# Kernel optimization log

Measured on AMD Instinct MI355X. Metric: run time of the kernel, lower is better.

Reference implementation:

```python
import jax, jax.numpy as jnp
import numpy as np

N = 200000
E = 500000
F_IN = 165
HID = 256
N_CLASSES = 2


def setup_inputs() -> dict:
    key = jax.random.key(0)
    ks = jax.random.split(key, 8)
    x = jax.random.normal(ks[0], (N, F_IN), dtype=jnp.float32)
    edge_index = jax.random.randint(ks[1], (2, E), 0, N, dtype=jnp.int64)
    # PyG SAGEConv params: lin_l applied to mean-aggregated neighbors (with bias),
    # lin_r applied to root features (no bias). Glorot-ish init scale.
    def lin(k, fin, fout):
        return jax.random.normal(k, (fin, fout), dtype=jnp.float32) / np.sqrt(fin)
    return {
        "x": x,
        "edge_index": edge_index,
        "w1_l": lin(ks[2], F_IN, HID),
        "w1_r": lin(ks[3], F_IN, HID),
        "b1": jnp.zeros((HID,), dtype=jnp.float32),
        "w2_l": lin(ks[4], HID, N_CLASSES),
        "w2_r": lin(ks[5], HID, N_CLASSES),
        "b2": jnp.zeros((N_CLASSES,), dtype=jnp.float32),
    }


def _sage_conv(x, edge_index, w_l, w_r, b):
    # PyG SAGEConv with default mean aggregation:
    #   out = lin_l(mean_{j in N(i)} x_j) + lin_r(x_i) + b
    src, dst = edge_index[0], edge_index[1]
    n = x.shape[0]
    deg = jax.ops.segment_sum(jnp.ones((src.shape[0],), x.dtype), dst, num_segments=n)
    agg = jax.ops.segment_sum(x[src], dst, num_segments=n)  # [N, F]
    agg = agg / jnp.maximum(deg, 1.0)[:, None]
    return agg @ w_l + x @ w_r + b


def reference(x, edge_index, w1_l, w1_r, b1, w2_l, w2_r, b2):
    h = jax.nn.relu(_sage_conv(x, edge_index, w1_l, w1_r, b1))
    # F.dropout(training=self.training) is identity in eval mode.
    logits = _sage_conv(h, edge_index, w2_l, w2_r, b2)
    return (logits, edge_index)
```

## Files before the change

### kernel.cpp

```cpp
#include <hip/hip_runtime.h>
#include <hip/hip_bf16.h>
#include <hip/hip_fp16.h>

#define N_NODES 200000
#define N_EDGES 500000
#define F_IN    165
#define HID     256
#define SX      192
#define NB      782

typedef float    floatx4 __attribute__((ext_vector_type(4)));
typedef float    floatx4a __attribute__((ext_vector_type(4), aligned(16)));
typedef float    float4u __attribute__((ext_vector_type(4), aligned(4)));
typedef _Float16 half8   __attribute__((ext_vector_type(8)));

__global__ void cast_x_kernel(const float* __restrict__ x, half8* __restrict__ xh8) {
    int idx = blockIdx.x * blockDim.x + threadIdx.x;
    int row = idx / 24;
    int p = idx - row * 24;
    int f0 = p * 8;
    const float* px = x + (long)row * F_IN + f0;
    half8 r;
    if (f0 + 8 <= F_IN) {
        float4u lo = *(const float4u*)px;
        float4u hi = *(const float4u*)(px + 4);
#pragma unroll
        for (int q = 0; q < 4; ++q) r[q] = (_Float16)lo[q];
#pragma unroll
        for (int q = 0; q < 4; ++q) r[4 + q] = (_Float16)hi[q];
    } else {
#pragma unroll
        for (int q = 0; q < 8; ++q)
            r[q] = (f0 + q < F_IN) ? (_Float16)px[q] : (_Float16)0.0f;
    }
    xh8[idx] = r;
}

__global__ void hist_kernel(const int* __restrict__ ei, int* __restrict__ degi) {
    int e = blockIdx.x * blockDim.x + threadIdx.x;
    if (e < N_EDGES) atomicAdd(&degi[ei[N_EDGES + e]], 1);
}

__global__ __launch_bounds__(256) void block_sum_kernel(const int* __restrict__ degi,
                                                        int* __restrict__ bsum) {
    __shared__ int sh[256];
    int t = threadIdx.x, i = blockIdx.x * 256 + t;
    sh[t] = (i < N_NODES) ? degi[i] : 0;
    __syncthreads();
#pragma unroll
    for (int off = 128; off > 0; off >>= 1) {
        if (t < off) sh[t] += sh[t + off];
        __syncthreads();
    }
    if (t == 0) bsum[blockIdx.x] = sh[0];
}

__global__ __launch_bounds__(1024) void scan_bsum_kernel(const int* __restrict__ bsum,
                                                         int* __restrict__ boff,
                                                         int* __restrict__ row_start) {
    __shared__ int sh[1024];
    int t = threadIdx.x;
    int v = (t < NB) ? bsum[t] : 0;
    sh[t] = v;
    __syncthreads();
    for (int off = 1; off < 1024; off <<= 1) {
        int u = (t >= off) ? sh[t - off] : 0;
        __syncthreads();
        sh[t] += u;
        __syncthreads();
    }
    if (t < NB) boff[t] = sh[t] - v;
    if (t == 1023) row_start[N_NODES] = sh[1023];
}

__global__ __launch_bounds__(256) void scan_emit_kernel(const int* __restrict__ degi,
                                                        const int* __restrict__ boff,
                                                        int* __restrict__ row_start,
                                                        int* __restrict__ cursor,
                                                        float* __restrict__ invdeg) {
    __shared__ int sh[256];
    int t = threadIdx.x, i = blockIdx.x * 256 + t;
    int d = (i < N_NODES) ? degi[i] : 0;
    sh[t] = d;
    __syncthreads();
#pragma unroll
    for (int off = 1; off < 256; off <<= 1) {
        int u = (t >= off) ? sh[t - off] : 0;
        __syncthreads();
        sh[t] += u;
        __syncthreads();
    }
    if (i < N_NODES) {
        int row = boff[blockIdx.x] + sh[t] - d;
        row_start[i] = row;
        cursor[i] = row;
        invdeg[i] = 1.0f / fmaxf((float)d, 1.0f);
    }
}

__global__ void scatter_edges_kernel(const int* __restrict__ ei,
                                     int* __restrict__ cursor,
                                     int* __restrict__ csr) {
    int e = blockIdx.x * blockDim.x + threadIdx.x;
    if (e >= N_EDGES) return;
    int s = ei[e];
    int d = ei[N_EDGES + e];
    int pos = atomicAdd(&cursor[d], 1);
    csr[pos] = s;
}

__global__ void gather_agg_kernel(const half8* __restrict__ xh8,
                                  const int* __restrict__ row_start,
                                  const int* __restrict__ csr,
                                  half8* __restrict__ aggh8) {
    int idx = blockIdx.x * blockDim.x + threadIdx.x;
    int n = idx / 24;
    int p = idx - n * 24;
    int e0 = row_start[n], e1 = row_start[n + 1];
    half8 acc = {0, 0, 0, 0, 0, 0, 0, 0};
    half8 acc2 = {0, 0, 0, 0, 0, 0, 0, 0};
    int e = e0;
    for (; e + 2 <= e1; e += 2) {
        int s0 = csr[e], s1 = csr[e + 1];
        half8 v0 = xh8[(long)s0 * 24 + p];
        half8 v1 = xh8[(long)s1 * 24 + p];
        acc += v0;
        acc2 += v1;
    }
    if (e < e1) acc += xh8[(long)csr[e] * 24 + p];
    aggh8[idx] = acc + acc2;
}

__global__ void prep_bfrag_kernel(const float* __restrict__ w1l,
                                  const float* __restrict__ w1r,
                                  _Float16* __restrict__ bfrag) {
    int gid = blockIdx.x * blockDim.x + threadIdx.x;
    if (gid >= 12 * 16 * 64) return;
    int lane = gid & 63;
    int j = (gid >> 6) & 15;
    int c = gid >> 10;
    int quad = lane >> 4, n = lane & 15;
    const float* w = (c < 6) ? w1l : w1r;
    int kb = (c < 6 ? c : c - 6) * 32;
    int col = j * 16 + n;
    half8 r;
#pragma unroll
    for (int q = 0; q < 8; ++q) {
        int k = kb + quad * 8 + q;
        r[q] = (_Float16)((k < F_IN) ? w[k * HID + col] : 0.0f);
    }
    *(half8*)(bfrag + gid * 8) = r;
}

__global__ __launch_bounds__(512, 2) void gemm_fused_kernel(
        const _Float16* __restrict__ xh, const _Float16* __restrict__ aggh,
        const float* __restrict__ invdeg, const _Float16* __restrict__ bfrag,
        const float* __restrict__ b1,
        const float* __restrict__ w2l, const float* __restrict__ w2r,
        float* __restrict__ tl, float* __restrict__ tr) {
    __shared__ __attribute__((aligned(16))) _Float16 As[2][128 * 32];
    __shared__ float tlr[128][4];
    const int tid = threadIdx.x;
    const int w = tid >> 6, lane = tid & 63;
    const int quad = lane >> 4, l15 = lane & 15;
    const int rowbase = blockIdx.x * 128;
    const int mrow0 = rowbase + (w & 1) * 64;
    const int rhalf = (w & 1) * 64;
    const int jbase = (w >> 1) * 4;

    ((float*)tlr)[tid < 512 ? tid : 0] = 0.0f;

    const int srow_l = tid >> 2;
    const int sseg = (tid & 3) ^ ((srow_l >> 1) & 3);
    int srow = rowbase + srow_l;
    if (srow >= N_NODES) srow = N_NODES - 1;
    const long sgoff = (long)srow * SX + sseg * 8;

    floatx4 acc[4][4];
#pragma unroll
    for (int i = 0; i < 4; ++i)
#pragma unroll
        for (int jj = 0; jj < 4; ++jj)
            acc[i][jj] = (floatx4){0.f, 0.f, 0.f, 0.f};

    __syncthreads();

#pragma unroll 1
    for (int it = 0; it < 6; ++it) {
#pragma unroll
        for (int u = 0; u < 2; ++u) {
            const int cc = it * 2 + u;
            const _Float16* __restrict__ src = (cc < 6) ? aggh : xh;
            const int kb = (cc < 6 ? cc : cc - 6) * 32;
            const _Float16* gp = src + sgoff + kb;
            char* dst = (char*)(&As[u][0]) + (tid & ~63) * 16;
            __builtin_amdgcn_global_load_lds(
                (const __attribute__((address_space(1))) void*)gp,
                (__attribute__((address_space(3))) void*)dst, 16, 0, 0);
        }
        __syncthreads();

#pragma unroll
        for (int u = 0; u < 2; ++u) {
            const int cc = it * 2 + u;
            half8 a[4], b[4];
#pragma unroll
            for (int i = 0; i < 4; ++i) {
                int r = rhalf + i * 16 + l15;
                int slot = r * 4 + (quad ^ ((r >> 1) & 3));
                a[i] = *(const half8*)(&As[u][slot * 8]);
            }
#pragma unroll
            for (int jj = 0; jj < 4; ++jj)
                b[jj] = *(const half8*)(bfrag + (((cc * 16) + jbase + jj) * 64 + lane) * 8);
#pragma unroll
            for (int i = 0; i < 4; ++i)
#pragma unroll
                for (int jj = 0; jj < 4; ++jj)
                    acc[i][jj] = __builtin_amdgcn_mfma_f32_16x16x32_f16(a[i], b[jj], acc[i][jj], 0, 0, 0);

            if (cc == 5) {
#pragma unroll
                for (int i = 0; i < 4; ++i) {
                    int rb = mrow0 + i * 16 + quad * 4;
                    floatx4 iv;
                    if (rb + 3 < N_NODES) {
                        iv = *(const floatx4a*)(invdeg + rb);
                    } else {
#pragma unroll
                        for (int t = 0; t < 4; ++t)
                            iv[t] = (rb + t < N_NODES) ? invdeg[rb + t] : 0.0f;
                    }
#pragma unroll
                    for (int jj = 0; jj < 4; ++jj)
                        acc[i][jj] *= iv;
                }
            }
        }
        __syncthreads();
    }

    float bb[4], wl0[4], wl1[4], wr0[4], wr1[4];
#pragma unroll
    for (int jj = 0; jj < 4; ++jj) {
        int col = (w >> 1) * 64 + jj * 16 + l15;
        bb[jj]  = b1[col];
        wl0[jj] = w2l[col * 2];  wl1[jj] = w2l[col * 2 + 1];
        wr0[jj] = w2r[col * 2];  wr1[jj] = w2r[col * 2 + 1];
    }
#pragma unroll
    for (int i = 0; i < 4; ++i) {
#pragma unroll
        for (int t = 0; t < 4; ++t) {
            float s0 = 0.f, s1 = 0.f, s2 = 0.f, s3 = 0.f;
#pragma unroll
            for (int jj = 0; jj < 4; ++jj) {
                float v = fmaxf(acc[i][jj][t] + bb[jj], 0.0f);
                s0 += v * wl0[jj]; s1 += v * wl1[jj];
                s2 += v * wr0[jj]; s3 += v * wr1[jj];
            }
#pragma unroll
            for (int m = 1; m < 16; m <<= 1) {
                s0 += __shfl_xor(s0, m, 64);
                s1 += __shfl_xor(s1, m, 64);
                s2 += __shfl_xor(s2, m, 64);
                s3 += __shfl_xor(s3, m, 64);
            }
            if (l15 == 0) {
                int rl = (w & 1) * 64 + i * 16 + quad * 4 + t;
                atomicAdd(&tlr[rl][0], s0);
                atomicAdd(&tlr[rl][1], s1);
                atomicAdd(&tlr[rl][2], s2);
                atomicAdd(&tlr[rl][3], s3);
            }
        }
    }
    __syncthreads();
    if (tid < 128) {
        int row = rowbase + tid;
        if (row < N_NODES) {
            tl[row * 2 + 0] = tlr[tid][0];
            tl[row * 2 + 1] = tlr[tid][1];
            tr[row * 2 + 0] = tlr[tid][2];
            tr[row * 2 + 1] = tlr[tid][3];
        }
    }
}

__global__ void gather_out_kernel(const int* __restrict__ row_start,
                                  const int* __restrict__ csr,
                                  const float* __restrict__ tl,
                                  const float* __restrict__ tr,
                                  const float* __restrict__ invdeg,
                                  const float* __restrict__ b2,
                                  float* __restrict__ out) {
    int i = blockIdx.x * blockDim.x + threadIdx.x;
    if (i >= N_NODES) return;
    int e0 = row_start[i], e1 = row_start[i + 1];
    float a0 = 0.f, a1 = 0.f;
    for (int e = e0; e < e1; ++e) {
        int s = csr[e];
        a0 += tl[s * 2 + 0];
        a1 += tl[s * 2 + 1];
    }
    float inv = invdeg[i];
    out[i * 2 + 0] = a0 * inv + tr[i * 2 + 0] + b2[0];
    out[i * 2 + 1] = a1 * inv + tr[i * 2 + 1] + b2[1];
}

__global__ void cast_edges_kernel(const int* __restrict__ ei,
                                  float* __restrict__ out) {
    int i = blockIdx.x * blockDim.x + threadIdx.x;
    if (i < 2 * N_EDGES) out[i] = (float)ei[i];
}

extern "C" void kernel_launch(void* const* d_in, const int* in_sizes, int n_in,
                              void* d_out, int out_size, void* d_ws, size_t ws_size,
                              hipStream_t stream) {
    const float* x    = (const float*)d_in[0];
    const int*   ei   = (const int*)d_in[1];
    const float* w1_l = (const float*)d_in[2];
    const float* w1_r = (const float*)d_in[3];
    const float* b1   = (const float*)d_in[4];
    const float* w2_l = (const float*)d_in[5];
    const float* w2_r = (const float*)d_in[6];
    const float* b2   = (const float*)d_in[7];

    char* ws = (char*)d_ws;
    int*   degi      = (int*)(ws);
    int*   row_start = (int*)(ws + 800000);
    int*   cursor    = (int*)(ws + 1600032);
    float* invdeg    = (float*)(ws + 2400032);
    int*   csr       = (int*)(ws + 3200032);
    float* tl        = (float*)(ws + 5200032);
    float* tr        = (float*)(ws + 6800032);
    int*   bsum      = (int*)(ws + 8400032);
    int*   boff      = (int*)(ws + 8403232);
    _Float16* bfrag  = (_Float16*)(ws + 8406432);
    _Float16* aggh   = (_Float16*)(ws + 8610000);
    _Float16* xh     = (_Float16*)(ws + 85410000);

    float* out = (float*)d_out;

    (void)hipMemsetAsync(degi, 0, 800000, stream);

    cast_x_kernel<<<(N_NODES * 24) / 256, 256, 0, stream>>>(x, (half8*)xh);
    prep_bfrag_kernel<<<48, 256, 0, stream>>>(w1_l, w1_r, bfrag);

    hist_kernel<<<(N_EDGES + 255) / 256, 256, 0, stream>>>(ei, degi);
    block_sum_kernel<<<NB, 256, 0, stream>>>(degi, bsum);
    scan_bsum_kernel<<<1, 1024, 0, stream>>>(bsum, boff, row_start);
    scan_emit_kernel<<<NB, 256, 0, stream>>>(degi, boff, row_start, cursor, invdeg);
    scatter_edges_kernel<<<(N_EDGES + 255) / 256, 256, 0, stream>>>(ei, cursor, csr);

    gather_agg_kernel<<<(N_NODES * 24) / 256, 256, 0, stream>>>(
        (const half8*)xh, row_start, csr, (half8*)aggh);

    gemm_fused_kernel<<<(N_NODES + 127) / 128, 512, 0, stream>>>(
        xh, aggh, invdeg, bfrag, b1, w2_l, w2_r, tl, tr);

    gather_out_kernel<<<NB, 256, 0, stream>>>(row_start, csr, tl, tr, invdeg, b2, out);
    cast_edges_kernel<<<(2 * N_EDGES + 255) / 256, 256, 0, stream>>>(ei, out + 2 * N_NODES);
}
```

Baseline: 424.8 us.

## Fuse prep kernels, replace scan with atomic wave offsets, double-buffer GEMM loads

Merges the x cast, degree histogram and weight-fragment prep into one kernel, and merges the output gather with the edge cast. The three-kernel prefix scan is replaced by a per-wave shuffle scan that claims its base offset with a global atomic, so CSR rows are no longer in node order and row end is taken from degree. The GEMM now double-buffers its LDS tiles, issuing the next tile's loads before computing on the current one. Together these cut launch count and overlap GEMM memory traffic with compute, at the cost of doubled LDS use and nondeterministic CSR layout.

Measured after the change: 477.0 us. 1.12x slower.

```diff
diff --git a/kernel.cpp b/kernel.cpp
--- a/kernel.cpp
+++ b/kernel.cpp
@@ -14,86 +14,72 @@
 typedef float    float4u __attribute__((ext_vector_type(4), aligned(4)));
 typedef _Float16 half8   __attribute__((ext_vector_type(8)));
 
-__global__ void cast_x_kernel(const float* __restrict__ x, half8* __restrict__ xh8) {
+__global__ void prep_kernel(const float* __restrict__ x, half8* __restrict__ xh8,
+                            const int* __restrict__ ei, int* __restrict__ degi,
+                            const float* __restrict__ w1l, const float* __restrict__ w1r,
+                            _Float16* __restrict__ bfrag) {
     int idx = blockIdx.x * blockDim.x + threadIdx.x;
-    int row = idx / 24;
-    int p = idx - row * 24;
-    int f0 = p * 8;
-    const float* px = x + (long)row * F_IN + f0;
-    half8 r;
-    if (f0 + 8 <= F_IN) {
-        float4u lo = *(const float4u*)px;
-        float4u hi = *(const float4u*)(px + 4);
-#pragma unroll
-        for (int q = 0; q < 4; ++q) r[q] = (_Float16)lo[q];
-#pragma unroll
-        for (int q = 0; q < 4; ++q) r[4 + q] = (_Float16)hi[q];
-    } else {
-#pragma unroll
-        for (int q = 0; q < 8; ++q)
-            r[q] = (f0 + q < F_IN) ? (_Float16)px[q] : (_Float16)0.0f;
-    }
-    xh8[idx] = r;
-}
-
-__global__ void hist_kernel(const int* __restrict__ ei, int* __restrict__ degi) {
-    int e = blockIdx.x * blockDim.x + threadIdx.x;
-    if (e < N_EDGES) atomicAdd(&degi[ei[N_EDGES + e]], 1);
-}
-
-__global__ __launch_bounds__(256) void block_sum_kernel(const int* __restrict__ degi,
-                                                        int* __restrict__ bsum) {
-    __shared__ int sh[256];
-    int t = threadIdx.x, i = blockIdx.x * 256 + t;
-    sh[t] = (i < N_NODES) ? degi[i] : 0;
-    __syncthreads();
-#pragma unroll
-    for (int off = 128; off > 0; off >>= 1) {
-        if (t < off) sh[t] += sh[t + off];
-        __syncthreads();
-    }
-    if (t == 0) bsum[blockIdx.x] = sh[0];
-}
-
-__global__ __launch_bounds__(1024) void scan_bsum_kernel(const int* __restrict__ bsum,
-                                                         int* __restrict__ boff,
-                                                         int* __restrict__ row_start) {
-    __shared__ int sh[1024];
-    int t = threadIdx.x;
-    int v = (t < NB) ? bsum[t] : 0;
-    sh[t] = v;
-    __syncthreads();
-    for (int off = 1; off < 1024; off <<= 1) {
-        int u = (t >= off) ? sh[t - off] : 0;
-        __syncthreads();
-        sh[t] += u;
-        __syncthreads();
-    }
-    if (t < NB) boff[t] = sh[t] - v;
-    if (t == 1023) row_start[N_NODES] = sh[1023];
-}
-
-__global__ __launch_bounds__(256) void scan_emit_kernel(const int* __restrict__ degi,
-                                                        const int* __restrict__ boff,
-                                                        int* __restrict__ row_start,
-                                                        int* __restrict__ cursor,
-                                                        float* __restrict__ invdeg) {
-    __shared__ int sh[256];
-    int t = threadIdx.x, i = blockIdx.x * 256 + t;
+    {
+        int row = idx / 24;
+        int p = idx - row * 24;
+        int f0 = p * 8;
+        const float* px = x + (long)row * F_IN + f0;
+        half8 r;
+        if (f0 + 8 <= F_IN) {
+            float4u lo = *(const float4u*)px;
+            float4u hi = *(const float4u*)(px + 4);
+#pragma unroll
+            for (int q = 0; q < 4; ++q) r[q] = (_Float16)lo[q];
+#pragma unroll
+            for (int q = 0; q < 4; ++q) r[4 + q] = (_Float16)hi[q];
+        } else {
+#pragma unroll
+            for (int q = 0; q < 8; ++q)
+                r[q] = (f0 + q < F_IN) ? (_Float16)px[q] : (_Float16)0.0f;
+        }
+        xh8[idx] = r;
+    }
+    if (idx < N_EDGES) atomicAdd(&degi[ei[N_EDGES + idx]], 1);
+    int gid = idx - (1 << 20);
+    if ((unsigned)gid < (unsigned)(12 * 16 * 64)) {
+        int lane = gid & 63;
+        int j = (gid >> 6) & 15;
+        int c = gid >> 10;
+        int quad = lane >> 4, n = lane & 15;
+        const float* w = (c < 6) ? w1l : w1r;
+        int kb = (c < 6 ? c : c - 6) * 32;
+        int col = j * 16 + n;
+        half8 r;
+#pragma unroll
+        for (int q = 0; q < 8; ++q) {
+            int k = kb + quad * 8 + q;
+            r[q] = (_Float16)((k < F_IN) ? w[k * HID + col] : 0.0f);
+        }
+        *(half8*)(bfrag + gid * 8) = r;
+    }
+}
+
+__global__ __launch_bounds__(256) void region_kernel(const int* __restrict__ degi,
+                                                     int* __restrict__ row_start,
+                                                     int* __restrict__ cursor,
+                                                     float* __restrict__ invdeg,
+                                                     int* __restrict__ gctr) {
+    int i = blockIdx.x * 256 + threadIdx.x;
+    int lane = threadIdx.x & 63;
     int d = (i < N_NODES) ? degi[i] : 0;
-    sh[t] = d;
-    __syncthreads();
-#pragma unroll
-    for (int off = 1; off < 256; off <<= 1) {
-        int u = (t >= off) ? sh[t - off] : 0;
-        __syncthreads();
-        sh[t] += u;
-        __syncthreads();
-    }
+    int pre = d;
+#pragma unroll
+    for (int m = 1; m < 64; m <<= 1) {
+        int u = __shfl_up(pre, m, 64);
+        if (lane >= m) pre += u;
+    }
+    int base = 0;
+    if (lane == 63) base = atomicAdd(gctr, pre);
+    base = __shfl(base, 63, 64);
     if (i < N_NODES) {
-        int row = boff[blockIdx.x] + sh[t] - d;
-        row_start[i] = row;
-        cursor[i] = row;
+        int rs = base + pre - d;
+        row_start[i] = rs;
+        cursor[i] = rs;
         invdeg[i] = 1.0f / fmaxf((float)d, 1.0f);
     }
 }
@@ -111,12 +97,13 @@
 
 __global__ void gather_agg_kernel(const half8* __restrict__ xh8,
                                   const int* __restrict__ row_start,
+                                  const int* __restrict__ degi,
                                   const int* __restrict__ csr,
                                   half8* __restrict__ aggh8) {
     int idx = blockIdx.x * blockDim.x + threadIdx.x;
     int n = idx / 24;
     int p = idx - n * 24;
-    int e0 = row_start[n], e1 = row_start[n + 1];
+    int e0 = row_start[n], e1 = e0 + degi[n];
     half8 acc = {0, 0, 0, 0, 0, 0, 0, 0};
     half8 acc2 = {0, 0, 0, 0, 0, 0, 0, 0};
     int e = e0;
@@ -131,34 +118,13 @@
     aggh8[idx] = acc + acc2;
 }
 
-__global__ void prep_bfrag_kernel(const float* __restrict__ w1l,
-                                  const float* __restrict__ w1r,
-                                  _Float16* __restrict__ bfrag) {
-    int gid = blockIdx.x * blockDim.x + threadIdx.x;
-    if (gid >= 12 * 16 * 64) return;
-    int lane = gid & 63;
-    int j = (gid >> 6) & 15;
-    int c = gid >> 10;
-    int quad = lane >> 4, n = lane & 15;
-    const float* w = (c < 6) ? w1l : w1r;
-    int kb = (c < 6 ? c : c - 6) * 32;
-    int col = j * 16 + n;
-    half8 r;
-#pragma unroll
-    for (int q = 0; q < 8; ++q) {
-        int k = kb + quad * 8 + q;
-        r[q] = (_Float16)((k < F_IN) ? w[k * HID + col] : 0.0f);
-    }
-    *(half8*)(bfrag + gid * 8) = r;
-}
-
 __global__ __launch_bounds__(512, 2) void gemm_fused_kernel(
         const _Float16* __restrict__ xh, const _Float16* __restrict__ aggh,
         const float* __restrict__ invdeg, const _Float16* __restrict__ bfrag,
         const float* __restrict__ b1,
         const float* __restrict__ w2l, const float* __restrict__ w2r,
         float* __restrict__ tl, float* __restrict__ tr) {
-    __shared__ __attribute__((aligned(16))) _Float16 As[2][128 * 32];
+    __shared__ __attribute__((aligned(16))) _Float16 As[2][128 * 64];
     __shared__ float tlr[128][4];
     const int tid = threadIdx.x;
     const int w = tid >> 6, lane = tid & 63;
@@ -168,7 +134,7 @@
     const int rhalf = (w & 1) * 64;
     const int jbase = (w >> 1) * 4;
 
-    ((float*)tlr)[tid < 512 ? tid : 0] = 0.0f;
+    ((float*)tlr)[tid] = 0.0f;
 
     const int srow_l = tid >> 2;
     const int sseg = (tid & 3) ^ ((srow_l >> 1) & 3);
@@ -183,32 +149,45 @@
         for (int jj = 0; jj < 4; ++jj)
             acc[i][jj] = (floatx4){0.f, 0.f, 0.f, 0.f};
 
-    __syncthreads();
-
-#pragma unroll 1
-    for (int it = 0; it < 6; ++it) {
+#pragma unroll
+    for (int u = 0; u < 2; ++u) {
+        const int cc = u;
+        const _Float16* __restrict__ src = (cc < 6) ? aggh : xh;
+        const int kb = (cc < 6 ? cc : cc - 6) * 32;
+        const _Float16* gp = src + sgoff + kb;
+        char* dst = (char*)(&As[0][u * 128 * 32]) + (tid & ~63) * 16;
+        __builtin_amdgcn_global_load_lds(
+            (const __attribute__((address_space(1))) void*)gp,
+            (__attribute__((address_space(3))) void*)dst, 16, 0, 0);
+    }
+    asm volatile("s_waitcnt vmcnt(0)" ::: "memory");
+    __builtin_amdgcn_s_barrier();
+    __builtin_amdgcn_sched_barrier(0);
+
+#pragma unroll
+    for (int t = 0; t < 6; ++t) {
+        if (t < 5) {
+#pragma unroll
+            for (int u = 0; u < 2; ++u) {
+                const int cc = (t + 1) * 2 + u;
+                const _Float16* __restrict__ src = (cc < 6) ? aggh : xh;
+                const int kb = (cc < 6 ? cc : cc - 6) * 32;
+                const _Float16* gp = src + sgoff + kb;
+                char* dst = (char*)(&As[(t + 1) & 1][u * 128 * 32]) + (tid & ~63) * 16;
+                __builtin_amdgcn_global_load_lds(
+                    (const __attribute__((address_space(1))) void*)gp,
+                    (__attribute__((address_space(3))) void*)dst, 16, 0, 0);
+            }
+        }
 #pragma unroll
         for (int u = 0; u < 2; ++u) {
-            const int cc = it * 2 + u;
-            const _Float16* __restrict__ src = (cc < 6) ? aggh : xh;
-            const int kb = (cc < 6 ? cc : cc - 6) * 32;
-            const _Float16* gp = src + sgoff + kb;
-            char* dst = (char*)(&As[u][0]) + (tid & ~63) * 16;
-            __builtin_amdgcn_global_load_lds(
-                (const __attribute__((address_space(1))) void*)gp,
-                (__attribute__((address_space(3))) void*)dst, 16, 0, 0);
-        }
-        __syncthreads();
-
-#pragma unroll
-        for (int u = 0; u < 2; ++u) {
-            const int cc = it * 2 + u;
+            const int cc = t * 2 + u;
             half8 a[4], b[4];
 #pragma unroll
             for (int i = 0; i < 4; ++i) {
                 int r = rhalf + i * 16 + l15;
                 int slot = r * 4 + (quad ^ ((r >> 1) & 3));
-                a[i] = *(const half8*)(&As[u][slot * 8]);
+                a[i] = *(const half8*)(&As[t & 1][u * 128 * 32 + slot * 8]);
             }
 #pragma unroll
             for (int jj = 0; jj < 4; ++jj)
@@ -228,8 +207,8 @@
                         iv = *(const floatx4a*)(invdeg + rb);
                     } else {
 #pragma unroll
-                        for (int t = 0; t < 4; ++t)
-                            iv[t] = (rb + t < N_NODES) ? invdeg[rb + t] : 0.0f;
+                        for (int q = 0; q < 4; ++q)
+                            iv[q] = (rb + q < N_NODES) ? invdeg[rb + q] : 0.0f;
                     }
 #pragma unroll
                     for (int jj = 0; jj < 4; ++jj)
@@ -237,7 +216,9 @@
                 }
             }
         }
-        __syncthreads();
+        asm volatile("s_waitcnt vmcnt(0)" ::: "memory");
+        __builtin_amdgcn_s_barrier();
+        __builtin_amdgcn_sched_barrier(0);
     }
 
     float bb[4], wl0[4], wl1[4], wr0[4], wr1[4];
@@ -251,11 +232,11 @@
 #pragma unroll
     for (int i = 0; i < 4; ++i) {
 #pragma unroll
-        for (int t = 0; t < 4; ++t) {
+        for (int q = 0; q < 4; ++q) {
             float s0 = 0.f, s1 = 0.f, s2 = 0.f, s3 = 0.f;
 #pragma unroll
             for (int jj = 0; jj < 4; ++jj) {
-                float v = fmaxf(acc[i][jj][t] + bb[jj], 0.0f);
+                float v = fmaxf(acc[i][jj][q] + bb[jj], 0.0f);
                 s0 += v * wl0[jj]; s1 += v * wl1[jj];
                 s2 += v * wr0[jj]; s3 += v * wr1[jj];
             }
@@ -267,7 +248,7 @@
                 s3 += __shfl_xor(s3, m, 64);
             }
             if (l15 == 0) {
-                int rl = (w & 1) * 64 + i * 16 + quad * 4 + t;
+                int rl = (w & 1) * 64 + i * 16 + quad * 4 + q;
                 atomicAdd(&tlr[rl][0], s0);
                 atomicAdd(&tlr[rl][1], s1);
                 atomicAdd(&tlr[rl][2], s2);
@@ -287,31 +268,29 @@
     }
 }
 
-__global__ void gather_out_kernel(const int* __restrict__ row_start,
-                                  const int* __restrict__ csr,
-                                  const float* __restrict__ tl,
-                                  const float* __restrict__ tr,
-                                  const float* __restrict__ invdeg,
-                                  const float* __restrict__ b2,
-                                  float* __restrict__ out) {
+__global__ void out_kernel(const int* __restrict__ row_start,
+                           const int* __restrict__ degi,
+                           const int* __restrict__ csr,
+                           const float* __restrict__ tl,
+                           const float* __restrict__ tr,
+                           const float* __restrict__ invdeg,
+                           const float* __restrict__ b2,
+                           const int* __restrict__ ei,
+                           float* __restrict__ out) {
     int i = blockIdx.x * blockDim.x + threadIdx.x;
-    if (i >= N_NODES) return;
-    int e0 = row_start[i], e1 = row_start[i + 1];
-    float a0 = 0.f, a1 = 0.f;
-    for (int e = e0; e < e1; ++e) {
-        int s = csr[e];
-        a0 += tl[s * 2 + 0];
-        a1 += tl[s * 2 + 1];
-    }
-    float inv = invdeg[i];
-    out[i * 2 + 0] = a0 * inv + tr[i * 2 + 0] + b2[0];
-    out[i * 2 + 1] = a1 * inv + tr[i * 2 + 1] + b2[1];
-}
-
-__global__ void cast_edges_kernel(const int* __restrict__ ei,
-                                  float* __restrict__ out) {
-    int i = blockIdx.x * blockDim.x + threadIdx.x;
-    if (i < 2 * N_EDGES) out[i] = (float)ei[i];
+    if (i < N_NODES) {
+        int e0 = row_start[i], e1 = e0 + degi[i];
+        float a0 = 0.f, a1 = 0.f;
+        for (int e = e0; e < e1; ++e) {
+            int s = csr[e];
+            a0 += tl[s * 2 + 0];
+            a1 += tl[s * 2 + 1];
+        }
+        float inv = invdeg[i];
+        out[i * 2 + 0] = a0 * inv + tr[i * 2 + 0] + b2[0];
+        out[i * 2 + 1] = a1 * inv + tr[i * 2 + 1] + b2[1];
+    }
+    if (i < 2 * N_EDGES) out[2 * N_NODES + i] = (float)ei[i];
 }
 
 extern "C" void kernel_launch(void* const* d_in, const int* in_sizes, int n_in,
@@ -334,8 +313,7 @@
     int*   csr       = (int*)(ws + 3200032);
     float* tl        = (float*)(ws + 5200032);
     float* tr        = (float*)(ws + 6800032);
-    int*   bsum      = (int*)(ws + 8400032);
-    int*   boff      = (int*)(ws + 8403232);
+    int*   gctr      = (int*)(ws + 8400032);
     _Float16* bfrag  = (_Float16*)(ws + 8406432);
     _Float16* aggh   = (_Float16*)(ws + 8610000);
     _Float16* xh     = (_Float16*)(ws + 85410000);
@@ -343,22 +321,20 @@
     float* out = (float*)d_out;
 
     (void)hipMemsetAsync(degi, 0, 800000, stream);
-
-    cast_x_kernel<<<(N_NODES * 24) / 256, 256, 0, stream>>>(x, (half8*)xh);
-    prep_bfrag_kernel<<<48, 256, 0, stream>>>(w1_l, w1_r, bfrag);
-
-    hist_kernel<<<(N_EDGES + 255) / 256, 256, 0, stream>>>(ei, degi);
-    block_sum_kernel<<<NB, 256, 0, stream>>>(degi, bsum);
-    scan_bsum_kernel<<<1, 1024, 0, stream>>>(bsum, boff, row_start);
-    scan_emit_kernel<<<NB, 256, 0, stream>>>(degi, boff, row_start, cursor, invdeg);
+    (void)hipMemsetAsync(gctr, 0, 4, stream);
+
+    prep_kernel<<<(N_NODES * 24) / 256, 256, 0, stream>>>(
+        x, (half8*)xh, ei, degi, w1_l, w1_r, bfrag);
+
+    region_kernel<<<NB, 256, 0, stream>>>(degi, row_start, cursor, invdeg, gctr);
     scatter_edges_kernel<<<(N_EDGES + 255) / 256, 256, 0, stream>>>(ei, cursor, csr);
 
     gather_agg_kernel<<<(N_NODES * 24) / 256, 256, 0, stream>>>(
-        (const half8*)xh, row_start, csr, (half8*)aggh);
+        (const half8*)xh, row_start, degi, csr, (half8*)aggh);
 
     gemm_fused_kernel<<<(N_NODES + 127) / 128, 512, 0, stream>>>(
         xh, aggh, invdeg, bfrag, b1, w2_l, w2_r, tl, tr);
 
-    gather_out_kernel<<<NB, 256, 0, stream>>>(row_start, csr, tl, tr, invdeg, b2, out);
-    cast_edges_kernel<<<(2 * N_EDGES + 255) / 256, 256, 0, stream>>>(ei, out + 2 * N_NODES);
-}
+    out_kernel<<<(2 * N_EDGES + 255) / 256, 256, 0, stream>>>(
+        row_start, degi, csr, tl, tr, invdeg, b2, ei, out);
+}
```
